# Kernel optimization log

Hardware: AMD Instinct MI355X
Metric: run time of the kernel (lower is better)

Reference implementation:

```python
import jax, jax.numpy as jnp
import numpy as np

D_MODEL = 1024
N_HEADS = 16
THETA = 10000.0


def _rope(x, token_positions):
    # x: (b, h, s, d_k); token_positions: (b, s)
    d_k = x.shape[-1]
    powers = jnp.arange(0, d_k, 2, dtype=jnp.float32) / d_k        # (d_k/2,)
    freqs = 1.0 / (THETA ** powers)
    ang = token_positions.astype(jnp.float32)[..., None] * freqs   # (b, s, d_k/2)
    cos = jnp.cos(ang)[:, None, :, :].astype(x.dtype)              # (b, 1, s, d_k/2)
    sin = jnp.sin(ang)[:, None, :, :].astype(x.dtype)
    x_even = x[..., ::2]
    x_odd = x[..., 1::2]
    r1 = x_even * cos - x_odd * sin
    r2 = x_even * sin + x_odd * cos
    # interleave back to (..., d_k)
    return jnp.stack([r1, r2], axis=-1).reshape(x.shape)


def reference(x, token_positions, wq, wk, wv, wo):
    B, S, D = x.shape
    H = N_HEADS
    d_k = D // H

    def proj(w):
        y = jnp.einsum('bsi,oi->bso', x, w)
        return y.reshape(B, S, H, d_k).transpose(0, 2, 1, 3)  # (b, h, s, d_k)

    q = _rope(proj(wq), token_positions)
    k = _rope(proj(wk), token_positions)
    v = proj(wv)

    scale = 1.0 / jnp.sqrt(jnp.asarray(d_k, dtype=x.dtype))
    score = jnp.einsum('bhqd,bhkd->bhqk', q, k) * scale  # (b, h, s, s)
    causal = jnp.tril(jnp.ones((S, S), dtype=bool))
    score = jnp.where(causal, score, -jnp.inf)
    probs = jax.nn.softmax(score, axis=-1)
    attn = jnp.einsum('bhqk,bhkd->bhqd', probs, v)
    attn = attn.transpose(0, 2, 1, 3).reshape(B, S, D)
    return jnp.einsum('bsi,oi->bso', attn, wo)


def setup_inputs() -> dict:
    key = jax.random.key(0)
    ks = jax.random.split(key, 6)
    B, S, D = 2, 2048, D_MODEL
    std = (2.0 / (D + D)) ** 0.5
    x = jax.random.normal(ks[0], (B, S, D), dtype=jnp.float32)
    token_positions = jnp.broadcast_to(jnp.arange(S, dtype=jnp.int32), (B, S))
    wq = jax.random.normal(ks[1], (D, D), dtype=jnp.float32) * std
    wk = jax.random.normal(ks[2], (D, D), dtype=jnp.float32) * std
    wv = jax.random.normal(ks[3], (D, D), dtype=jnp.float32) * std
    wo = jax.random.normal(ks[4], (D, D), dtype=jnp.float32) * std
    return {"x": x, "token_positions": token_positions, "wq": wq, "wk": wk, "wv": wv, "wo": wo}
```

## Files before the change

### kernel.cpp

```cpp
#include <hip/hip_runtime.h>
#include <hip/hip_bf16.h>

typedef unsigned short u16;
typedef unsigned int u32;
typedef short short8 __attribute__((ext_vector_type(8)));
typedef u16 u16x8 __attribute__((ext_vector_type(8)));
typedef u16 u16x4 __attribute__((ext_vector_type(4)));
typedef u32 u32x4 __attribute__((ext_vector_type(4)));
typedef float f32x4 __attribute__((ext_vector_type(4)));
typedef float f32x16 __attribute__((ext_vector_type(16)));

#define MFMA(a, b, c) __builtin_amdgcn_mfma_f32_16x16x32_bf16((a), (b), (c), 0, 0, 0)
#define MFMA32(a, b, c) __builtin_amdgcn_mfma_f32_32x32x16_bf16((a), (b), (c), 0, 0, 0)

#define QSCALE 0.18033688011112042f

__device__ __forceinline__ u16 f2bf(float f) {
  unsigned u = __float_as_uint(f);
  unsigned r = (u + 0x7fffu + ((u >> 16) & 1u)) >> 16;
  return (u16)r;
}
__device__ __forceinline__ float bf2f(u16 h) {
  return __uint_as_float(((unsigned)h) << 16);
}
__device__ __forceinline__ float exp2hw(float x) {
  float r;
  asm("v_exp_f32 %0, %1" : "=v"(r) : "v"(x));
  return r;
}
__device__ __forceinline__ u32 cvtpk(float lo, float hi) {
  u32 d;
  asm("v_cvt_pk_bf16_f32 %0, %1, %2" : "=v"(d) : "v"(lo), "v"(hi));
  return d;
}
__device__ __forceinline__ float max3f(float a, float b, float c) {
  float d;
  asm("v_max3_f32 %0, %1, %2, %3" : "=v"(d) : "v"(a), "v"(b), "v"(c));
  return d;
}
__device__ __forceinline__ void plswap(u32& a, u32& b) {
  asm volatile("v_permlane32_swap_b32 %0, %1" : "+v"(a), "+v"(b));
}
__device__ __forceinline__ void async16(const void* g, void* l) {
  __builtin_amdgcn_global_load_lds(
      (const __attribute__((address_space(1))) void*)g,
      (__attribute__((address_space(3))) void*)l, 16, 0, 0);
}
__device__ __forceinline__ f32x16 zero16() {
  f32x16 z;
#pragma unroll
  for (int i = 0; i < 16; i++) z[i] = 0.f;
  return z;
}
#define WAITV(N) asm volatile("s_waitcnt vmcnt(" #N ")" ::: "memory")
#define WAITL0() asm volatile("s_waitcnt lgkmcnt(0)" ::: "memory")
#define BAR() __builtin_amdgcn_s_barrier()
#define PRIO1 __builtin_amdgcn_s_setprio(1)
#define PRIO0 __builtin_amdgcn_s_setprio(0)

__global__ __launch_bounds__(256) void convert_kernel(
    const float* __restrict__ x, const float* __restrict__ wq,
    const float* __restrict__ wk, const float* __restrict__ wv,
    const float* __restrict__ wo, u16* __restrict__ ws,
    const int* __restrict__ tp, float* __restrict__ tab) {
  int blk = blockIdx.x;
  if (blk >= 4096) {
    int t = (blk - 4096) * 256 + threadIdx.x;
    int bs = t >> 5, p = t & 31;
    float freq = exp2hw(-(float)p * 0.4152410118609203f);
    float ang = (float)tp[bs] * freq;
    float sn, cs;
    sincosf(ang, &sn, &cs);
    tab[bs * 64 + p * 2] = cs;
    tab[bs * 64 + p * 2 + 1] = sn;
    return;
  }
  const float* src; u16* dst;
  if (blk < 2048)      { src = x;  dst = ws; }
  else if (blk < 2560) { src = wq; dst = ws + 4194304;               blk -= 2048; }
  else if (blk < 3072) { src = wk; dst = ws + 4194304 + 1048576;     blk -= 2560; }
  else if (blk < 3584) { src = wv; dst = ws + 4194304 + 2 * 1048576; blk -= 3072; }
  else                 { src = wo; dst = ws + 4194304 + 3 * 1048576; blk -= 3584; }
  int idx = (blk * 256 + threadIdx.x) * 8;
  float4 v0 = *(const float4*)(src + idx);
  float4 v1 = *(const float4*)(src + idx + 4);
  u16x8 o;
  o[0] = f2bf(v0.x); o[1] = f2bf(v0.y); o[2] = f2bf(v0.z); o[3] = f2bf(v0.w);
  o[4] = f2bf(v1.x); o[5] = f2bf(v1.y); o[6] = f2bf(v1.z); o[7] = f2bf(v1.w);
  *(u16x8*)(dst + idx) = o;
}

__global__ __launch_bounds__(512, 2) void gemm_qkv256(
    const u16* __restrict__ xb, const u16* __restrict__ Wg,
    const float* __restrict__ tab, u16* __restrict__ qb, u16* __restrict__ kb,
    u16* __restrict__ vt) {
  __shared__ u16 As[2][16384];
  __shared__ u16 Bs[2][12288];
  const int tid = threadIdx.x, lane = tid & 63, wid = tid >> 6;
  const int wm = wid >> 2, wn = wid & 3;
  const int g = lane >> 4, r = lane & 15;
  const int lid = ((blockIdx.x & 7) << 5) + (blockIdx.x >> 3);
  const int rowBase = (lid >> 4) << 8;
  const int colBase = (lid & 15) * 192;

#define STG_A(BUF, T)                                                         \
  do {                                                                        \
    _Pragma("unroll") for (int i_ = 0; i_ < 4; ++i_) {                        \
      int c = i_ * 512 + tid;                                                 \
      int row = c >> 3, kc = ((c & 7) ^ (row & 7)) * 8;                       \
      async16(xb + (size_t)(rowBase + row) * 1024 + (T)*64 + kc,              \
              (char*)As[BUF] + c * 16);                                       \
    }                                                                         \
  } while (0)
#define STG_B(BUF, T)                                                         \
  do {                                                                        \
    _Pragma("unroll") for (int i_ = 0; i_ < 3; ++i_) {                        \
      int c = i_ * 512 + tid;                                                 \
      int row = c >> 3, kc = ((c & 7) ^ (row & 7)) * 8;                       \
      async16(Wg + (size_t)(colBase + row) * 1024 + (T)*64 + kc,              \
              (char*)Bs[BUF] + c * 16);                                       \
    }                                                                         \
  } while (0)

  f32x4 acc[8][3];
#pragma unroll
  for (int m = 0; m < 8; m++)
#pragma unroll
    for (int n = 0; n < 3; n++) acc[m][n] = (f32x4){0.f, 0.f, 0.f, 0.f};
  short8 af[4][2], bfr[3][2];

#define RD_A(CUR, MH)                                                         \
  do {                                                                        \
    _Pragma("unroll") for (int mi = 0; mi < 4; mi++) {                        \
      int ra = wm * 128 + (MH)*64 + mi * 16 + r;                              \
      const u16* p = As[CUR] + ra * 64;                                       \
      int sw = (ra & 7) << 3;                                                 \
      af[mi][0] = *(const short8*)(p + ((g << 3) ^ sw));                      \
      af[mi][1] = *(const short8*)(p + (((4 + g) << 3) ^ sw));                \
    }                                                                         \
  } while (0)
#define RD_B(CUR)                                                             \
  do {                                                                        \
    _Pragma("unroll") for (int ni = 0; ni < 3; ni++) {                        \
      int cb = wn * 48 + ni * 16 + r;                                         \
      const u16* p = Bs[CUR] + cb * 64;                                       \
      int sw = (cb & 7) << 3;                                                 \
      bfr[ni][0] = *(const short8*)(p + ((g << 3) ^ sw));                     \
      bfr[ni][1] = *(const short8*)(p + (((4 + g) << 3) ^ sw));               \
    }                                                                         \
  } while (0)
#define MM24(MH)                                                              \
  do {                                                                        \
    _Pragma("unroll") for (int mi = 0; mi < 4; mi++)                          \
        _Pragma("unroll") for (int ni = 0; ni < 3; ni++) {                    \
      acc[(MH)*4 + mi][ni] = MFMA(af[mi][0], bfr[ni][0], acc[(MH)*4 + mi][ni]); \
      acc[(MH)*4 + mi][ni] = MFMA(af[mi][1], bfr[ni][1], acc[(MH)*4 + mi][ni]); \
    }                                                                         \
  } while (0)

  STG_A(0, 0); STG_B(0, 0);
  STG_A(1, 1);
  WAITV(4);
  BAR();

  for (int t = 0; t < 16; ++t) {
    const int cur = t & 1, nxt = cur ^ 1;
    RD_A(cur, 0);
    RD_B(cur);
    if (t < 15) STG_B(nxt, t + 1);
    BAR(); WAITL0();
    PRIO1; MM24(0); PRIO0; BAR();
    RD_A(cur, 1);
    if (t < 14) {
      STG_A(cur, t + 2);
      WAITV(4);
    } else {
      WAITV(0);
    }
    BAR(); WAITL0();
    PRIO1; MM24(1); PRIO0; BAR();
  }
#undef STG_A
#undef STG_B
#undef RD_A
#undef RD_B
#undef MM24

  const int colF = colBase + wn * 48;
#pragma unroll
  for (int n = 0; n < 3; n++) {
    const int col3 = colF + n * 16 + r;
    const int z = col3 >> 10;
    const int col = col3 & 1023;
    if (z < 2) {
      u16* dst = z ? kb : qb;
      const float qs = z ? 1.0f : QSCALE;
      const int p2 = (col >> 1) & 31;
      const bool odd = col & 1;
#pragma unroll
      for (int m = 0; m < 8; m++)
#pragma unroll
        for (int i = 0; i < 4; i++) {
          const int row = rowBase + wm * 128 + m * 16 + g * 4 + i;
          float2 cssn = *(const float2*)(tab + row * 64 + p2 * 2);
          float v = acc[m][n][i];
          float part = __shfl_xor(v, 1);
          float res = odd ? (part * cssn.y + v * cssn.x)
                          : (v * cssn.x - part * cssn.y);
          dst[(size_t)row * 1024 + col] = f2bf(res * qs);
        }
    } else {
#pragma unroll
      for (int m = 0; m < 8; m++)
#pragma unroll
        for (int i = 0; i < 4; i++) {
          const int row = rowBase + wm * 128 + m * 16 + g * 4 + i;
          const int bb = row >> 11, s = row & 2047;
          vt[(size_t)((bb * 16 + (col >> 6)) * 64 + (col & 63)) * 2048 + s] =
              f2bf(acc[m][n][i]);
        }
    }
  }
}


__global__ __launch_bounds__(256, 4) void attn_kernel(
    const u16* __restrict__ qg, const u16* __restrict__ kg,
    const u16* __restrict__ vt, u16* __restrict__ p0, u16* __restrict__ p1,
    float* __restrict__ mbuf, float* __restrict__ lbuf) {
  __shared__ u16 Ks[2][64 * 64];
  __shared__ u16 Vs[2][64 * 64];
  const int tid = threadIdx.x, wid = tid >> 6, lane = tid & 63;
  const int q5 = lane & 31, hi = lane >> 5;
  const int akc = blockIdx.x >> 5, bh = blockIdx.x & 31;
  const int a = akc >> 2, k = (akc >> 1) & 1, c = akc & 1;
  const int b = bh >> 4, h = bh & 15;
  const int base = (wid < 2) ? a : (15 - a);
  const int rb = base * 128 + k * 64 + (wid & 1) * 32;
  const int cmax = rb >> 5;
  const int jend = 30 - 2 * a + k;
  const int qrow = (b << 11) + rb + q5;

  short8 bq[4];
  {
    const u16* qp = qg + (size_t)qrow * 1024 + (h << 6) + hi * 8;
    bq[0] = *(const short8*)(qp);
    bq[1] = *(const short8*)(qp + 16);
    bq[2] = *(const short8*)(qp + 32);
    bq[3] = *(const short8*)(qp + 48);
  }
  f32x16 accO0 = zero16(), accO1 = zero16();
  float m_r = -1e30f, l_r = 0.f;

#define STAGE(JT, BUF)                                                        \
  do {                                                                        \
    _Pragma("unroll") for (int i_ = 0; i_ < 2; i_++) {                        \
      int cc_ = i_ * 256 + tid;                                               \
      int row = cc_ >> 3, cc = (cc_ & 7) ^ (row & 7);                         \
      async16(kg + (size_t)((b << 11) + ((JT) << 6) + row) * 1024 +           \
                  (h << 6) + cc * 8,                                          \
              (char*)Ks[BUF] + cc_ * 16);                                     \
      async16(vt + (size_t)((bh << 6) + row) * 2048 + ((JT) << 6) + cc * 8,   \
              (char*)Vs[BUF] + cc_ * 16);                                     \
    }                                                                         \
  } while (0)

  if (c <= jend) STAGE(c, 0);

  for (int jj = c; jj <= jend; jj += 2) {
    const int cur = ((jj - c) >> 1) & 1;
    if (jj + 2 <= jend) {
      STAGE(jj + 2, cur ^ 1);
      WAITV(4);
    } else {
      WAITV(0);
    }
    BAR();
    if (2 * jj <= cmax) {
      const u16* Kb = Ks[cur];
      const u16* Vb = Vs[cur];
      const bool has1 = (2 * jj + 1 <= cmax);
      const int rsw = (q5 & 7) << 3;
      f32x16 s0 = zero16(), s1 = zero16();
      PRIO1;
#pragma unroll
      for (int kk = 0; kk < 4; kk++) {
        short8 kf =
            *(const short8*)(Kb + q5 * 64 + ((((kk << 1) + hi) << 3) ^ rsw));
        s0 = MFMA32(kf, bq[kk], s0);
      }
      PRIO0;
      if (has1) {
        PRIO1;
#pragma unroll
        for (int kk = 0; kk < 4; kk++) {
          short8 kf = *(const short8*)(Kb + (32 + q5) * 64 +
                                       ((((kk << 1) + hi) << 3) ^ rsw));
          s1 = MFMA32(kf, bq[kk], s1);
        }
        PRIO0;
      }
      if (2 * jj == cmax) {
#pragma unroll
        for (int rg = 0; rg < 16; rg++) {
          int rowk = (rg & 3) + 8 * (rg >> 2) + 4 * hi;
          if (rowk > q5) s0[rg] = -1e30f;
        }
      } else if (2 * jj + 1 == cmax) {
#pragma unroll
        for (int rg = 0; rg < 16; rg++) {
          int rowk = (rg & 3) + 8 * (rg >> 2) + 4 * hi;
          if (rowk > q5) s1[rg] = -1e30f;
        }
      }
      float pmax = max3f(s0[0], s0[1], s0[2]);
#pragma unroll
      for (int rg = 3; rg < 15; rg += 2) pmax = max3f(pmax, s0[rg], s0[rg + 1]);
      pmax = fmaxf(pmax, s0[15]);
      if (has1) {
#pragma unroll
        for (int rg = 0; rg < 16; rg += 2) pmax = max3f(pmax, s1[rg], s1[rg + 1]);
      }
      pmax = fmaxf(pmax, __shfl_xor(pmax, 32));
      if (!__all(pmax <= m_r + 8.0f)) {
        float mn = fmaxf(m_r, pmax);
        float sc = exp2hw(m_r - mn);
        l_r *= sc;
#pragma unroll
        for (int rg = 0; rg < 16; rg++) {
          accO0[rg] *= sc;
          accO1[rg] *= sc;
        }
        m_r = mn;
      }
      float rs = 0.f;
      u32 pw00[4], pw01[4], pw10[4], pw11[4];
#define PACK(SREG, OUT, S16)                                                  \
  do {                                                                        \
    float pp0 = exp2hw(SREG[(S16)*8 + 0] - m_r);                              \
    float pp1 = exp2hw(SREG[(S16)*8 + 1] - m_r);                              \
    float pp2 = exp2hw(SREG[(S16)*8 + 2] - m_r);                              \
    float pp3 = exp2hw(SREG[(S16)*8 + 3] - m_r);                              \
    float pp4 = exp2hw(SREG[(S16)*8 + 4] - m_r);                              \
    float pp5 = exp2hw(SREG[(S16)*8 + 5] - m_r);                              \
    float pp6 = exp2hw(SREG[(S16)*8 + 6] - m_r);                              \
    float pp7 = exp2hw(SREG[(S16)*8 + 7] - m_r);                              \
    rs += ((pp0 + pp1) + (pp2 + pp3)) + ((pp4 + pp5) + (pp6 + pp7));          \
    u32 X = cvtpk(pp0, pp1), Y = cvtpk(pp2, pp3);                             \
    u32 U = cvtpk(pp4, pp5), W = cvtpk(pp6, pp7);                             \
    plswap(X, U);                                                             \
    plswap(Y, W);                                                             \
    OUT[0] = X; OUT[1] = Y; OUT[2] = U; OUT[3] = W;                           \
  } while (0)
      PACK(s0, pw00, 0);
      PACK(s0, pw01, 1);
      if (has1) {
        PACK(s1, pw10, 0);
        PACK(s1, pw11, 1);
      }
#undef PACK
      rs += __shfl_xor(rs, 32);
      l_r += rs;
#define PVSTEP(PW, CH)                                                        \
  do {                                                                        \
    u32x4 pv_ = {PW[0], PW[1], PW[2], PW[3]};                                 \
    short8 pb_ = __builtin_bit_cast(short8, pv_);                             \
    short8 v0_ =                                                              \
        *(const short8*)(Vb + q5 * 64 + ((((CH) + hi) << 3) ^ rsw));          \
    short8 v1_ = *(const short8*)(Vb + (32 + q5) * 64 +                       \
                                  ((((CH) + hi) << 3) ^ rsw));                \
    accO0 = MFMA32(v0_, pb_, accO0);                                          \
    accO1 = MFMA32(v1_, pb_, accO1);                                          \
  } while (0)
      PRIO1;
      PVSTEP(pw00, 0);
      PVSTEP(pw01, 2);
      if (has1) {
        PVSTEP(pw10, 4);
        PVSTEP(pw11, 6);
      }
      PRIO0;
#undef PVSTEP
    }
    WAITL0();
    BAR();
  }
#undef STAGE

  u16* pout = c ? p1 : p0;
#pragma unroll
  for (int qd = 0; qd < 4; qd++) {
    u16x4 o0, o1;
#pragma unroll
    for (int e = 0; e < 4; e++) {
      o0[e] = f2bf(accO0[qd * 4 + e]);
      o1[e] = f2bf(accO1[qd * 4 + e]);
    }
    u16* op = pout + (size_t)qrow * 1024 + (h << 6) + qd * 8 + hi * 4;
    *(u16x4*)(op) = o0;
    *(u16x4*)(op + 32) = o1;
  }
  if (hi == 0) {
    int mli = c * 65536 + (bh << 11) + rb + q5;
    mbuf[mli] = m_r;
    lbuf[mli] = l_r;
  }
}

__global__ __launch_bounds__(256) void attn_merge(const u16* __restrict__ p1,
                                                  const float* __restrict__ mbuf,
                                                  const float* __restrict__ lbuf,
                                                  u16* __restrict__ ab) {
  int t = blockIdx.x * 256 + threadIdx.x;
  int dg = t & 7, row = t >> 3;
  int bh = row >> 11, s = row & 2047;
  int b = bh >> 4, h = bh & 15;
  size_t addr = (size_t)((b << 11) + s) * 1024 + (h << 6) + dg * 8;
  float m0 = mbuf[row], m1 = mbuf[65536 + row];
  float l0 = lbuf[row], l1 = lbuf[65536 + row];
  float m = fmaxf(m0, m1);
  float w0 = exp2hw(m0 - m), w1 = exp2hw(m1 - m);
  float inv = 1.0f / (l0 * w0 + l1 * w1);
  u16x8 o0 = *(const u16x8*)(ab + addr);
  u16x8 o1 = *(const u16x8*)(p1 + addr);
  u16x8 o;
#pragma unroll
  for (int i = 0; i < 8; i++)
    o[i] = f2bf((bf2f(o0[i]) * w0 + bf2f(o1[i]) * w1) * inv);
  *(u16x8*)(ab + addr) = o;
}

__global__ __launch_bounds__(512) void gemm_ao(const u16* __restrict__ ab,
                                               const u16* __restrict__ wob,
                                               float* __restrict__ out) {
  __shared__ u16 As[2][8192], Bs[2][8192];
  const int tid = threadIdx.x, lane = tid & 63, wid = tid >> 6;
  const int wm = wid >> 2, wn = wid & 3;
  const int g = lane >> 4, r = lane & 15;
  const int lid = ((blockIdx.x & 7) << 5) + (blockIdx.x >> 3);
  const int rowBase = (lid >> 3) << 7;
  const int colBase = (lid & 7) << 7;

#define AOSTG(KT, BUF)                                                        \
  do {                                                                        \
    _Pragma("unroll") for (int i_ = 0; i_ < 2; ++i_) {                        \
      int c = i_ * 512 + tid;                                                 \
      int row = c >> 3, kc = ((c & 7) ^ (row & 7)) * 8;                       \
      async16(ab + (size_t)(rowBase + row) * 1024 + ((KT) << 6) + kc,         \
              (char*)As[BUF] + c * 16);                                       \
    }                                                                         \
    _Pragma("unroll") for (int i_ = 0; i_ < 2; ++i_) {                        \
      int c = i_ * 512 + tid;                                                 \
      int row = c >> 3, kc = ((c & 7) ^ (row & 7)) * 8;                       \
      async16(wob + (size_t)(colBase + row) * 1024 + ((KT) << 6) + kc,        \
              (char*)Bs[BUF] + c * 16);                                       \
    }                                                                         \
  } while (0)

  f32x4 acc[4][2];
#pragma unroll
  for (int m = 0; m < 4; m++)
#pragma unroll
    for (int n = 0; n < 2; n++) acc[m][n] = (f32x4){0.f, 0.f, 0.f, 0.f};

  AOSTG(0, 0);
  for (int kt = 0; kt < 16; ++kt) {
    const int cur = kt & 1;
    if (kt + 1 < 16) {
      AOSTG(kt + 1, cur ^ 1);
      WAITV(4);
    } else {
      WAITV(0);
    }
    BAR();
    const u16* Ab = As[cur];
    const u16* Bb = Bs[cur];
    short8 af[4][2], bfr[2][2];
#pragma unroll
    for (int m = 0; m < 4; m++) {
      int ra = wm * 64 + m * 16 + r;
      const u16* p = Ab + ra * 64;
      int sw = (ra & 7) << 3;
      af[m][0] = *(const short8*)(p + ((g << 3) ^ sw));
      af[m][1] = *(const short8*)(p + (((4 + g) << 3) ^ sw));
    }
#pragma unroll
    for (int n = 0; n < 2; n++) {
      int cb = wn * 32 + n * 16 + r;
      const u16* p = Bb + cb * 64;
      int sw = (cb & 7) << 3;
      bfr[n][0] = *(const short8*)(p + ((g << 3) ^ sw));
      bfr[n][1] = *(const short8*)(p + (((4 + g) << 3) ^ sw));
    }
    PRIO1;
#pragma unroll
    for (int m = 0; m < 4; m++)
#pragma unroll
      for (int n = 0; n < 2; n++) {
        acc[m][n] = MFMA(af[m][0], bfr[n][0], acc[m][n]);
        acc[m][n] = MFMA(af[m][1], bfr[n][1], acc[m][n]);
      }
    PRIO0;
    WAITL0();
    BAR();
  }
#undef AOSTG

  const int rowB = rowBase + wm * 64;
  const int colB = colBase + wn * 32;
#pragma unroll
  for (int m = 0; m < 4; m++)
#pragma unroll
    for (int n = 0; n < 2; n++)
#pragma unroll
      for (int i = 0; i < 4; i++)
        out[(size_t)(rowB + m * 16 + g * 4 + i) * 1024 + colB + n * 16 + r] =
            acc[m][n][i];
}

extern "C" void kernel_launch(void* const* d_in, const int* in_sizes, int n_in,
                              void* d_out, int out_size, void* d_ws,
                              size_t ws_size, hipStream_t stream) {
  const float* x = (const float*)d_in[0];
  const int* tp = (const int*)d_in[1];
  const float* wq = (const float*)d_in[2];
  const float* wk = (const float*)d_in[3];
  const float* wv = (const float*)d_in[4];
  const float* wo = (const float*)d_in[5];
  float* out = (float*)d_out;

  u16* ws = (u16*)d_ws;
  u16* xb = ws;
  u16* wqb = xb + 4194304;
  u16* wkb = wqb + 1048576;
  u16* wvb = wkb + 1048576;
  u16* wob = wvb + 1048576;
  u16* qb = wob + 1048576;
  u16* kb = qb + 4194304;
  u16* vtb = kb + 4194304;
  u16* ab = vtb + 4194304;
  float* tab = (float*)ab;
  float* mbuf = (float*)wqb;
  float* lbuf = (float*)wkb;

  convert_kernel<<<4608, 256, 0, stream>>>(x, wq, wk, wv, wo, ws, tp, tab);
  gemm_qkv256<<<256, 512, 0, stream>>>(xb, wqb, tab, qb, kb, vtb);
  attn_kernel<<<1024, 256, 0, stream>>>(qb, kb, vtb, ab, xb, mbuf, lbuf);
  attn_merge<<<2048, 256, 0, stream>>>(xb, mbuf, lbuf, ab);
  gemm_ao<<<256, 512, 0, stream>>>(ab, wob, out);
}
```

Before: 104.8 us.

## Halve QKV GEMM row tile to 128 and simplify double-buffered pipeline

The fused QKV projection GEMM now uses 128-row tiles instead of 256, doubling the grid to 512 blocks, and shrinks the A shared buffer and per-wave accumulators to match. The split half-tile loop with staggered A/B prefetch is replaced by a simpler loop that prefetches the full next A and B tile, then computes the current one. The aim is better CU occupancy and load balance on a 256-CU part, at the cost of more re-reads of the weight matrix and less compute per load.

```diff
diff --git a/kernel.cpp b/kernel.cpp
--- a/kernel.cpp
+++ b/kernel.cpp
@@ -90,25 +90,25 @@
   *(u16x8*)(dst + idx) = o;
 }
 
-__global__ __launch_bounds__(512, 2) void gemm_qkv256(
+__global__ __launch_bounds__(512) void gemm_qkv256(
     const u16* __restrict__ xb, const u16* __restrict__ Wg,
     const float* __restrict__ tab, u16* __restrict__ qb, u16* __restrict__ kb,
     u16* __restrict__ vt) {
-  __shared__ u16 As[2][16384];
+  __shared__ u16 As[2][8192];
   __shared__ u16 Bs[2][12288];
   const int tid = threadIdx.x, lane = tid & 63, wid = tid >> 6;
   const int wm = wid >> 2, wn = wid & 3;
   const int g = lane >> 4, r = lane & 15;
-  const int lid = ((blockIdx.x & 7) << 5) + (blockIdx.x >> 3);
-  const int rowBase = (lid >> 4) << 8;
+  const int lid = ((blockIdx.x & 7) << 6) + (blockIdx.x >> 3);
+  const int rowBase = (lid >> 4) << 7;
   const int colBase = (lid & 15) * 192;
 
 #define STG_A(BUF, T)                                                         \
   do {                                                                        \
-    _Pragma("unroll") for (int i_ = 0; i_ < 4; ++i_) {                        \
+    _Pragma("unroll") for (int i_ = 0; i_ < 2; ++i_) {                        \
       int c = i_ * 512 + tid;                                                 \
       int row = c >> 3, kc = ((c & 7) ^ (row & 7)) * 8;                       \
-      async16(xb + (size_t)(rowBase + row) * 1024 + (T)*64 + kc,              \
+      async16(xb + (size_t)(rowBase + row) * 1024 + ((T) << 6) + kc,          \
               (char*)As[BUF] + c * 16);                                       \
     }                                                                         \
   } while (0)
@@ -117,74 +117,61 @@
     _Pragma("unroll") for (int i_ = 0; i_ < 3; ++i_) {                        \
       int c = i_ * 512 + tid;                                                 \
       int row = c >> 3, kc = ((c & 7) ^ (row & 7)) * 8;                       \
-      async16(Wg + (size_t)(colBase + row) * 1024 + (T)*64 + kc,              \
+      async16(Wg + (size_t)(colBase + row) * 1024 + ((T) << 6) + kc,          \
               (char*)Bs[BUF] + c * 16);                                       \
     }                                                                         \
   } while (0)
 
-  f32x4 acc[8][3];
-#pragma unroll
-  for (int m = 0; m < 8; m++)
+  f32x4 acc[4][3];
+#pragma unroll
+  for (int m = 0; m < 4; m++)
 #pragma unroll
     for (int n = 0; n < 3; n++) acc[m][n] = (f32x4){0.f, 0.f, 0.f, 0.f};
-  short8 af[4][2], bfr[3][2];
-
-#define RD_A(CUR, MH)                                                         \
-  do {                                                                        \
-    _Pragma("unroll") for (int mi = 0; mi < 4; mi++) {                        \
-      int ra = wm * 128 + (MH)*64 + mi * 16 + r;                              \
-      const u16* p = As[CUR] + ra * 64;                                       \
-      int sw = (ra & 7) << 3;                                                 \
-      af[mi][0] = *(const short8*)(p + ((g << 3) ^ sw));                      \
-      af[mi][1] = *(const short8*)(p + (((4 + g) << 3) ^ sw));                \
-    }                                                                         \
-  } while (0)
-#define RD_B(CUR)                                                             \
-  do {                                                                        \
-    _Pragma("unroll") for (int ni = 0; ni < 3; ni++) {                        \
-      int cb = wn * 48 + ni * 16 + r;                                         \
-      const u16* p = Bs[CUR] + cb * 64;                                       \
-      int sw = (cb & 7) << 3;                                                 \
-      bfr[ni][0] = *(const short8*)(p + ((g << 3) ^ sw));                     \
-      bfr[ni][1] = *(const short8*)(p + (((4 + g) << 3) ^ sw));               \
-    }                                                                         \
-  } while (0)
-#define MM24(MH)                                                              \
-  do {                                                                        \
-    _Pragma("unroll") for (int mi = 0; mi < 4; mi++)                          \
-        _Pragma("unroll") for (int ni = 0; ni < 3; ni++) {                    \
-      acc[(MH)*4 + mi][ni] = MFMA(af[mi][0], bfr[ni][0], acc[(MH)*4 + mi][ni]); \
-      acc[(MH)*4 + mi][ni] = MFMA(af[mi][1], bfr[ni][1], acc[(MH)*4 + mi][ni]); \
-    }                                                                         \
-  } while (0)
 
   STG_A(0, 0); STG_B(0, 0);
-  STG_A(1, 1);
-  WAITV(4);
-  BAR();
-
   for (int t = 0; t < 16; ++t) {
-    const int cur = t & 1, nxt = cur ^ 1;
-    RD_A(cur, 0);
-    RD_B(cur);
-    if (t < 15) STG_B(nxt, t + 1);
-    BAR(); WAITL0();
-    PRIO1; MM24(0); PRIO0; BAR();
-    RD_A(cur, 1);
-    if (t < 14) {
-      STG_A(cur, t + 2);
-      WAITV(4);
+    const int cur = t & 1;
+    if (t + 1 < 16) {
+      STG_A(cur ^ 1, t + 1);
+      STG_B(cur ^ 1, t + 1);
+      WAITV(5);
     } else {
       WAITV(0);
     }
-    BAR(); WAITL0();
-    PRIO1; MM24(1); PRIO0; BAR();
+    BAR();
+    const u16* Ab = As[cur];
+    const u16* Bb = Bs[cur];
+    short8 af[4][2], bfr[3][2];
+#pragma unroll
+    for (int m = 0; m < 4; m++) {
+      int ra = wm * 64 + m * 16 + r;
+      const u16* p = Ab + ra * 64;
+      int sw = (ra & 7) << 3;
+      af[m][0] = *(const short8*)(p + ((g << 3) ^ sw));
+      af[m][1] = *(const short8*)(p + (((4 + g) << 3) ^ sw));
+    }
+#pragma unroll
+    for (int n = 0; n < 3; n++) {
+      int cb = wn * 48 + n * 16 + r;
+      const u16* p = Bb + cb * 64;
+      int sw = (cb & 7) << 3;
+      bfr[n][0] = *(const short8*)(p + ((g << 3) ^ sw));
+      bfr[n][1] = *(const short8*)(p + (((4 + g) << 3) ^ sw));
+    }
+    PRIO1;
+#pragma unroll
+    for (int m = 0; m < 4; m++)
+#pragma unroll
+      for (int n = 0; n < 3; n++) {
+        acc[m][n] = MFMA(af[m][0], bfr[n][0], acc[m][n]);
+        acc[m][n] = MFMA(af[m][1], bfr[n][1], acc[m][n]);
+      }
+    PRIO0;
+    WAITL0();
+    BAR();
   }
 #undef STG_A
 #undef STG_B
-#undef RD_A
-#undef RD_B
-#undef MM24
 
   const int colF = colBase + wn * 48;
 #pragma unroll
@@ -198,10 +185,10 @@
       const int p2 = (col >> 1) & 31;
       const bool odd = col & 1;
 #pragma unroll
-      for (int m = 0; m < 8; m++)
+      for (int m = 0; m < 4; m++)
 #pragma unroll
         for (int i = 0; i < 4; i++) {
-          const int row = rowBase + wm * 128 + m * 16 + g * 4 + i;
+          const int row = rowBase + wm * 64 + m * 16 + g * 4 + i;
           float2 cssn = *(const float2*)(tab + row * 64 + p2 * 2);
           float v = acc[m][n][i];
           float part = __shfl_xor(v, 1);
@@ -211,10 +198,10 @@
         }
     } else {
 #pragma unroll
-      for (int m = 0; m < 8; m++)
+      for (int m = 0; m < 4; m++)
 #pragma unroll
         for (int i = 0; i < 4; i++) {
-          const int row = rowBase + wm * 128 + m * 16 + g * 4 + i;
+          const int row = rowBase + wm * 64 + m * 16 + g * 4 + i;
           const int bb = row >> 11, s = row & 2047;
           vt[(size_t)((bb * 16 + (col >> 6)) * 64 + (col & 63)) * 2048 + s] =
               f2bf(acc[m][n][i]);
@@ -222,7 +209,6 @@
     }
   }
 }
-
 
 __global__ __launch_bounds__(256, 4) void attn_kernel(
     const u16* __restrict__ qg, const u16* __restrict__ kg,
@@ -544,7 +530,7 @@
   float* lbuf = (float*)wkb;
 
   convert_kernel<<<4608, 256, 0, stream>>>(x, wq, wk, wv, wo, ws, tp, tab);
-  gemm_qkv256<<<256, 512, 0, stream>>>(xb, wqb, tab, qb, kb, vtb);
+  gemm_qkv256<<<512, 512, 0, stream>>>(xb, wqb, tab, qb, kb, vtb);
   attn_kernel<<<1024, 256, 0, stream>>>(qb, kb, vtb, ab, xb, mbuf, lbuf);
   attn_merge<<<2048, 256, 0, stream>>>(xb, mbuf, lbuf, ab);
   gemm_ao<<<256, 512, 0, stream>>>(ab, wob, out);
```

Result: slower. 115.9 us (+10.5%).
